# Kernel tuning notes

Measured on AMD Instinct MI355X. Metric: run time of the kernel, lower is better.

## Reference

```python
import jax, jax.numpy as jnp
import numpy as np
from jax import lax

MAX_DISP = 192
DOWNSAMPLE = 4
DEPTH = MAX_DISP // DOWNSAMPLE  # 48 disparity levels
B, C, H, W = 4, 512, 96, 320


def setup_inputs() -> dict:
    key = jax.random.key(0)
    k1, k2 = jax.random.split(key)
    left_features = jax.random.normal(k1, (B, C, H, W), dtype=jnp.float32)
    right_features = jax.random.normal(k2, (B, C, H, W), dtype=jnp.float32)
    return {"left_features": left_features, "right_features": right_features}


def _cost_volume(left, right):
    # cost[b, i, h, w] = mean_c left[b,c,h,w] * right[b,c,h,w-i]  for w >= i, else 0
    w_idx = jnp.arange(left.shape[3])

    def body(carry, i):
        r = jnp.roll(right, i, axis=3)            # right[..., w-i] (wrapped)
        corr = jnp.mean(left * r, axis=1)         # [B, H, W]
        corr = jnp.where(w_idx >= i, corr, jnp.float32(0.0))
        return carry, corr

    _, cost = lax.scan(body, None, jnp.arange(DEPTH))  # [D, B, H, W]
    return jnp.transpose(cost, (1, 0, 2, 3))           # [B, D, H, W]


def reference(left_features, right_features):
    return _cost_volume(left_features, right_features)
```

## Files before the change

kernel.cpp:

```cpp
#include <hip/hip_runtime.h>
#include <hip/hip_bf16.h>

#define B_ 4
#define C_ 512
#define H_ 96
#define W_ 320
#define D_ 48
#define HW_ (H_*W_)

#define KC 32
#define NCHUNK (C_/KC)
#define LCOLS 160
#define COLS 368
#define CSTR 72
#define BUFB (COLS*CSTR)
#define NT 320
#define NC4 (COLS/4)
#define NU (NC4*8)
#define SIT 3
#define EPS 168

typedef __attribute__((ext_vector_type(8))) short bf16x8;
typedef __attribute__((ext_vector_type(4))) float f32x4;

__device__ __forceinline__ unsigned cvt2(float lo, float hi) {
  union { __hip_bfloat162 h2; unsigned u; } u;
  u.h2 = __float22bfloat162_rn(make_float2(lo, hi));
  return u.u;
}
__device__ __forceinline__ int ldsoff(int col, int q) {
  return col * CSTR + (q << 3);
}

#define BAR() do { \
  asm volatile("s_waitcnt lgkmcnt(0)" ::: "memory"); \
  __builtin_amdgcn_sched_barrier(0); \
  __builtin_amdgcn_s_barrier(); \
  __builtin_amdgcn_sched_barrier(0); } while (0)

__global__ __launch_bounds__(NT, 4)
void cost_volume_mfma(const float* __restrict__ Lp,
                      const float* __restrict__ Rp,
                      float* __restrict__ out) {
  __shared__ __align__(16) char lds[2 * BUFB];
  const int tid = threadIdx.x;
  const int bid = blockIdx.x;
  const int half = bid & 1;
  const int bh = bid >> 1;
  const int b = bh / H_, h = bh % H_;
  const int wv = tid >> 6;
  const int lc = tid & 15;
  const int lg = (tid >> 4) & 3;
  const int mh0 = 2 * wv;
  const int m0 = 10 * half + mh0;

  const float* sp[SIT];
  int dstb[SIT];
  bool sact[SIT];
#pragma unroll
  for (int it = 0; it < SIT; ++it) {
    const int u = tid + NT * it;
    bool a = (u < NU);
    const int uc = a ? u : 0;
    const int c4 = uc % NC4;
    const int chq = uc / NC4;
    const int col = 4 * c4;
    int x;
    const float* basep;
    if (col < LCOLS) { x = 160 * half + col; basep = Lp; }
    else             { x = 160 * half - 48 + (col - LCOLS); basep = Rp; a = a && (x >= 0); }
    if (x < 0) x = 0;
    sp[it] = basep + ((size_t)(b * C_ + 4 * chq) * H_ + h) * W_ + x;
    dstb[it] = ldsoff(col, chq);
    sact[it] = a;
  }

  float4 sreg[SIT][4];

#define SLOAD() \
  _Pragma("unroll") for (int it = 0; it < SIT; ++it) { \
    if (sact[it]) { \
      _Pragma("unroll") for (int l = 0; l < 4; ++l) \
        sreg[it][l] = *(const float4*)(sp[it] + (size_t)l * HW_); \
    } \
    sp[it] += (size_t)KC * HW_; \
  }

#define SWRITE(bb) \
  _Pragma("unroll") for (int it = 0; it < SIT; ++it) if (sact[it]) { \
    char* p = lds + (bb) * BUFB + dstb[it]; \
    uint2 v; \
    v.x = cvt2(sreg[it][0].x, sreg[it][1].x); v.y = cvt2(sreg[it][2].x, sreg[it][3].x); \
    *(uint2*)(p) = v; \
    v.x = cvt2(sreg[it][0].y, sreg[it][1].y); v.y = cvt2(sreg[it][2].y, sreg[it][3].y); \
    *(uint2*)(p + CSTR) = v; \
    v.x = cvt2(sreg[it][0].z, sreg[it][1].z); v.y = cvt2(sreg[it][2].z, sreg[it][3].z); \
    *(uint2*)(p + 2 * CSTR) = v; \
    v.x = cvt2(sreg[it][0].w, sreg[it][1].w); v.y = cvt2(sreg[it][2].w, sreg[it][3].w); \
    *(uint2*)(p + 3 * CSTR) = v; \
  }

  const int aoff0 = ldsoff(16 * mh0 + lc, 2 * lg);
  const int aoff1 = ldsoff(16 * (mh0 + 1) + lc, 2 * lg);
  int boff[5];
  bool bval[5];
#pragma unroll
  for (int dnp = 0; dnp < 5; ++dnp) {
    const int jn = m0 + 1 - dnp;
    const int jloc = jn - 10 * half;
    boff[dnp] = ldsoff(208 + 16 * jloc + lc, 2 * lg);
    bval[dnp] = (jn >= 0);
  }

  union FragU { uint2 h[2]; bf16x8 v; };
#define FREAD(fr, base, off) do { FragU _f; \
  _f.h[0] = *(const uint2*)((base) + (off)); \
  _f.h[1] = *(const uint2*)((base) + (off) + 8); fr = _f.v; } while (0)

  f32x4 acc[2][4];
#pragma unroll
  for (int ml = 0; ml < 2; ++ml)
#pragma unroll
    for (int dn = 0; dn < 4; ++dn) acc[ml][dn] = (f32x4){0.f, 0.f, 0.f, 0.f};

  SLOAD();
  SWRITE(0);
  SLOAD();
  BAR();
#pragma unroll 2
  for (int k = 0; k < NCHUNK; ++k) {
    const char* base = lds + (k & 1) * BUFB;
    bf16x8 a0, a1;
    FREAD(a0, base, aoff0);
    FREAD(a1, base, aoff1);
    bf16x8 bf[5];
#pragma unroll
    for (int dnp = 0; dnp < 5; ++dnp)
      if (bval[dnp]) FREAD(bf[dnp], base, boff[dnp]);
#pragma unroll
    for (int dn = 0; dn < 4; ++dn) {
      if (bval[dn + 1])
        acc[0][dn] = __builtin_amdgcn_mfma_f32_16x16x32_bf16(a0, bf[dn + 1], acc[0][dn], 0, 0, 0);
      if (bval[dn])
        acc[1][dn] = __builtin_amdgcn_mfma_f32_16x16x32_bf16(a1, bf[dn], acc[1][dn], 0, 0, 0);
    }
    if (k < NCHUNK - 1) {
      SWRITE((k + 1) & 1);
      if (k < NCHUNK - 2) SLOAD();
      BAR();
    }
  }

  __syncthreads();
  float* ep = (float*)lds;
#pragma unroll
  for (int e = 0; e < (D_ * EPS + NT - 1) / NT; ++e) {
    const int i = tid + NT * e;
    if (i < D_ * EPS) ep[i] = 0.f;
  }
  __syncthreads();
  const float scale = 1.f / 512.f;
#pragma unroll
  for (int ml = 0; ml < 2; ++ml) {
    const int mh = mh0 + ml;
#pragma unroll
    for (int dn = 0; dn < 4; ++dn) {
      const int jn = m0 + ml - dn;
      if (jn >= 0) {
#pragma unroll
        for (int q = 0; q < 4; ++q) {
          const int i = 4 * lg + q;
          const int d = 16 * dn + i - lc;
          if (d >= 0 && d < D_)
            ep[d * EPS + 16 * mh + i] = acc[ml][dn][q] * scale;
        }
      }
    }
  }
  __syncthreads();
#pragma unroll
  for (int e = 0; e < 6; ++e) {
    const int u = tid + NT * e;
    const int d = u / 40, c4 = u % 40;
    const float4 v = *(const float4*)(ep + d * EPS + 4 * c4);
    float* o = out + (((size_t)b * D_ + d) * H_ + h) * W_ + 160 * half + 4 * c4;
    *(float4*)o = v;
  }
}

extern "C" void kernel_launch(void* const* d_in, const int* in_sizes, int n_in,
                              void* d_out, int out_size, void* d_ws, size_t ws_size,
                              hipStream_t stream) {
  const float* left  = (const float*)d_in[0];
  const float* right = (const float*)d_in[1];
  float* outp = (float*)d_out;
  cost_volume_mfma<<<dim3(B_ * H_ * 2), dim3(NT), 0, stream>>>(left, right, outp);
}
```

Baseline: 124.4 us.

## Double-buffer global prefetch registers to fetch two chunks ahead

Adds a second register staging set so global loads run two channel chunks ahead, alternating between two register buffers. The shared-memory write of the next chunk is moved before the MFMA work of the current chunk, and the launch bound drops from 4 to 3 blocks per CU to free registers. The aim is to hide more HBM latency in what is mostly a bandwidth-bound loop. In exchange, register pressure rises and fewer blocks may be resident per CU.

After: 154.6 us. 24.2% more time.

```diff
diff --git a/kernel.cpp b/kernel.cpp
--- a/kernel.cpp
+++ b/kernel.cpp
@@ -38,7 +38,7 @@
   __builtin_amdgcn_s_barrier(); \
   __builtin_amdgcn_sched_barrier(0); } while (0)
 
-__global__ __launch_bounds__(NT, 4)
+__global__ __launch_bounds__(NT, 3)
 void cost_volume_mfma(const float* __restrict__ Lp,
                       const float* __restrict__ Rp,
                       float* __restrict__ out) {
@@ -54,7 +54,8 @@
   const int mh0 = 2 * wv;
   const int m0 = 10 * half + mh0;
 
-  const float* sp[SIT];
+  const float* spA[SIT];
+  const float* spB[SIT];
   int dstb[SIT];
   bool sact[SIT];
 #pragma unroll
@@ -70,33 +71,34 @@
     if (col < LCOLS) { x = 160 * half + col; basep = Lp; }
     else             { x = 160 * half - 48 + (col - LCOLS); basep = Rp; a = a && (x >= 0); }
     if (x < 0) x = 0;
-    sp[it] = basep + ((size_t)(b * C_ + 4 * chq) * H_ + h) * W_ + x;
+    spA[it] = basep + ((size_t)(b * C_ + 4 * chq) * H_ + h) * W_ + x;
+    spB[it] = spA[it] + (size_t)2 * KC * HW_;
     dstb[it] = ldsoff(col, chq);
     sact[it] = a;
   }
 
-  float4 sreg[SIT][4];
-
-#define SLOAD() \
+  float4 srA[SIT][4], srB[SIT][4];
+
+#define SLOADX(sr, sp, ADVCH) \
   _Pragma("unroll") for (int it = 0; it < SIT; ++it) { \
     if (sact[it]) { \
       _Pragma("unroll") for (int l = 0; l < 4; ++l) \
-        sreg[it][l] = *(const float4*)(sp[it] + (size_t)l * HW_); \
+        sr[it][l] = *(const float4*)(sp[it] + (size_t)l * HW_); \
     } \
-    sp[it] += (size_t)KC * HW_; \
-  }
-
-#define SWRITE(bb) \
+    sp[it] += (size_t)(ADVCH) * KC * HW_; \
+  }
+
+#define SWRITEX(sr, bb) \
   _Pragma("unroll") for (int it = 0; it < SIT; ++it) if (sact[it]) { \
     char* p = lds + (bb) * BUFB + dstb[it]; \
     uint2 v; \
-    v.x = cvt2(sreg[it][0].x, sreg[it][1].x); v.y = cvt2(sreg[it][2].x, sreg[it][3].x); \
+    v.x = cvt2(sr[it][0].x, sr[it][1].x); v.y = cvt2(sr[it][2].x, sr[it][3].x); \
     *(uint2*)(p) = v; \
-    v.x = cvt2(sreg[it][0].y, sreg[it][1].y); v.y = cvt2(sreg[it][2].y, sreg[it][3].y); \
+    v.x = cvt2(sr[it][0].y, sr[it][1].y); v.y = cvt2(sr[it][2].y, sr[it][3].y); \
     *(uint2*)(p + CSTR) = v; \
-    v.x = cvt2(sreg[it][0].z, sreg[it][1].z); v.y = cvt2(sreg[it][2].z, sreg[it][3].z); \
+    v.x = cvt2(sr[it][0].z, sr[it][1].z); v.y = cvt2(sr[it][2].z, sr[it][3].z); \
     *(uint2*)(p + 2 * CSTR) = v; \
-    v.x = cvt2(sreg[it][0].w, sreg[it][1].w); v.y = cvt2(sreg[it][2].w, sreg[it][3].w); \
+    v.x = cvt2(sr[it][0].w, sr[it][1].w); v.y = cvt2(sr[it][2].w, sr[it][3].w); \
     *(uint2*)(p + 3 * CSTR) = v; \
   }
 
@@ -123,12 +125,23 @@
 #pragma unroll
     for (int dn = 0; dn < 4; ++dn) acc[ml][dn] = (f32x4){0.f, 0.f, 0.f, 0.f};
 
-  SLOAD();
-  SWRITE(0);
-  SLOAD();
+  SLOADX(srA, spA, 1);
+  SWRITEX(srA, 0);
+  SLOADX(srA, spA, 2);
+  SLOADX(srB, spB, 2);
   BAR();
+
 #pragma unroll 2
   for (int k = 0; k < NCHUNK; ++k) {
+    if (k < NCHUNK - 1) {
+      if ((k & 1) == 0) {
+        SWRITEX(srA, (k + 1) & 1);
+        if (k < NCHUNK - 3) SLOADX(srA, spA, 2);
+      } else {
+        SWRITEX(srB, (k + 1) & 1);
+        if (k < NCHUNK - 3) SLOADX(srB, spB, 2);
+      }
+    }
     const char* base = lds + (k & 1) * BUFB;
     bf16x8 a0, a1;
     FREAD(a0, base, aoff0);
@@ -144,11 +157,7 @@
       if (bval[dn])
         acc[1][dn] = __builtin_amdgcn_mfma_f32_16x16x32_bf16(a1, bf[dn], acc[1][dn], 0, 0, 0);
     }
-    if (k < NCHUNK - 1) {
-      SWRITE((k + 1) & 1);
-      if (k < NCHUNK - 2) SLOAD();
-      BAR();
-    }
+    if (k < NCHUNK - 1) BAR();
   }
 
   __syncthreads();
```

## Split each row into single-wave blocks with private LDS windows and no barriers

Applied to the files above, without the earlier changes.

Each block is now one 64-thread wave that owns a 32-column output tile, up from 320-thread blocks each covering half a row. The launch grows to ten blocks per (batch, row). Each wave stages its own left tile plus the 80-column right window it needs into a single LDS buffer, so the double buffer and the workgroup barriers go away. The aim is more resident waves and no cross-wave synchronisation. The cost is that right-feature columns are loaded redundantly by neighbouring tiles, raising global/L2 traffic, and there is less explicit load/compute overlap per wave.

Measured after the change: 142.3 us. 1.14x slower.

```diff
diff --git a/kernel.cpp b/kernel.cpp
--- a/kernel.cpp
+++ b/kernel.cpp
@@ -10,15 +10,13 @@
 
 #define KC 32
 #define NCHUNK (C_/KC)
-#define LCOLS 160
-#define COLS 368
+#define WCOLS 112
 #define CSTR 72
-#define BUFB (COLS*CSTR)
-#define NT 320
-#define NC4 (COLS/4)
-#define NU (NC4*8)
-#define SIT 3
-#define EPS 168
+#define LDSB (WCOLS*CSTR)
+#define NT 64
+#define NUW 224
+#define SIT 4
+#define EPS2 36
 
 typedef __attribute__((ext_vector_type(8))) short bf16x8;
 typedef __attribute__((ext_vector_type(4))) float f32x4;
@@ -32,45 +30,41 @@
   return col * CSTR + (q << 3);
 }
 
-#define BAR() do { \
-  asm volatile("s_waitcnt lgkmcnt(0)" ::: "memory"); \
-  __builtin_amdgcn_sched_barrier(0); \
-  __builtin_amdgcn_s_barrier(); \
-  __builtin_amdgcn_sched_barrier(0); } while (0)
-
-__global__ __launch_bounds__(NT, 4)
+__global__ __launch_bounds__(NT)
 void cost_volume_mfma(const float* __restrict__ Lp,
                       const float* __restrict__ Rp,
                       float* __restrict__ out) {
-  __shared__ __align__(16) char lds[2 * BUFB];
-  const int tid = threadIdx.x;
+  __shared__ __align__(16) char lds[LDSB];
+  const int ln = threadIdx.x;
   const int bid = blockIdx.x;
-  const int half = bid & 1;
-  const int bh = bid >> 1;
+  const int t2 = bid % 10;
+  const int bh = bid / 10;
   const int b = bh / H_, h = bh % H_;
-  const int wv = tid >> 6;
-  const int lc = tid & 15;
-  const int lg = (tid >> 4) & 3;
-  const int mh0 = 2 * wv;
-  const int m0 = 10 * half + mh0;
+  const int lc = ln & 15;
+  const int lg = (ln >> 4) & 3;
+  const int m0 = 2 * t2;
 
   const float* sp[SIT];
   int dstb[SIT];
   bool sact[SIT];
 #pragma unroll
   for (int it = 0; it < SIT; ++it) {
-    const int u = tid + NT * it;
-    bool a = (u < NU);
+    const int u = ln + 64 * it;
+    bool a = (u < NUW);
     const int uc = a ? u : 0;
-    const int c4 = uc % NC4;
-    const int chq = uc / NC4;
+    const int c4 = uc % 28, chq = uc / 28;
     const int col = 4 * c4;
     int x;
-    const float* basep;
-    if (col < LCOLS) { x = 160 * half + col; basep = Lp; }
-    else             { x = 160 * half - 48 + (col - LCOLS); basep = Rp; a = a && (x >= 0); }
+    const float* bp;
+    if (c4 < 8) { x = 16 * m0 + col; bp = Lp; }
+    else {
+      const int dnp = (c4 - 8) >> 2, jn = m0 + 1 - dnp;
+      x = 16 * jn + 4 * ((c4 - 8) & 3);
+      bp = Rp;
+      a = a && (jn >= 0);
+    }
     if (x < 0) x = 0;
-    sp[it] = basep + ((size_t)(b * C_ + 4 * chq) * H_ + h) * W_ + x;
+    sp[it] = bp + ((size_t)(b * C_ + 4 * chq) * H_ + h) * W_ + x;
     dstb[it] = ldsoff(col, chq);
     sact[it] = a;
   }
@@ -86,9 +80,9 @@
     sp[it] += (size_t)KC * HW_; \
   }
 
-#define SWRITE(bb) \
+#define SWRITE() \
   _Pragma("unroll") for (int it = 0; it < SIT; ++it) if (sact[it]) { \
-    char* p = lds + (bb) * BUFB + dstb[it]; \
+    char* p = lds + dstb[it]; \
     uint2 v; \
     v.x = cvt2(sreg[it][0].x, sreg[it][1].x); v.y = cvt2(sreg[it][2].x, sreg[it][3].x); \
     *(uint2*)(p) = v; \
@@ -100,22 +94,20 @@
     *(uint2*)(p + 3 * CSTR) = v; \
   }
 
-  const int aoff0 = ldsoff(16 * mh0 + lc, 2 * lg);
-  const int aoff1 = ldsoff(16 * (mh0 + 1) + lc, 2 * lg);
+  const int aoff0 = ldsoff(lc, 2 * lg);
+  const int aoff1 = ldsoff(16 + lc, 2 * lg);
   int boff[5];
   bool bval[5];
 #pragma unroll
   for (int dnp = 0; dnp < 5; ++dnp) {
-    const int jn = m0 + 1 - dnp;
-    const int jloc = jn - 10 * half;
-    boff[dnp] = ldsoff(208 + 16 * jloc + lc, 2 * lg);
-    bval[dnp] = (jn >= 0);
+    boff[dnp] = ldsoff(32 + 16 * dnp + lc, 2 * lg);
+    bval[dnp] = (m0 + 1 - dnp) >= 0;
   }
 
   union FragU { uint2 h[2]; bf16x8 v; };
-#define FREAD(fr, base, off) do { FragU _f; \
-  _f.h[0] = *(const uint2*)((base) + (off)); \
-  _f.h[1] = *(const uint2*)((base) + (off) + 8); fr = _f.v; } while (0)
+#define FREAD(fr, off) do { FragU _f; \
+  _f.h[0] = *(const uint2*)(lds + (off)); \
+  _f.h[1] = *(const uint2*)(lds + (off) + 8); fr = _f.v; } while (0)
 
   f32x4 acc[2][4];
 #pragma unroll
@@ -124,19 +116,16 @@
     for (int dn = 0; dn < 4; ++dn) acc[ml][dn] = (f32x4){0.f, 0.f, 0.f, 0.f};
 
   SLOAD();
-  SWRITE(0);
+  SWRITE();
   SLOAD();
-  BAR();
-#pragma unroll 2
   for (int k = 0; k < NCHUNK; ++k) {
-    const char* base = lds + (k & 1) * BUFB;
     bf16x8 a0, a1;
-    FREAD(a0, base, aoff0);
-    FREAD(a1, base, aoff1);
+    FREAD(a0, aoff0);
+    FREAD(a1, aoff1);
     bf16x8 bf[5];
 #pragma unroll
     for (int dnp = 0; dnp < 5; ++dnp)
-      if (bval[dnp]) FREAD(bf[dnp], base, boff[dnp]);
+      if (bval[dnp]) FREAD(bf[dnp], boff[dnp]);
 #pragma unroll
     for (int dn = 0; dn < 4; ++dn) {
       if (bval[dn + 1])
@@ -144,35 +133,30 @@
       if (bval[dn])
         acc[1][dn] = __builtin_amdgcn_mfma_f32_16x16x32_bf16(a1, bf[dn], acc[1][dn], 0, 0, 0);
     }
-    if (k < NCHUNK - 1) {
-      SWRITE((k + 1) & 1);
-      if (k < NCHUNK - 2) SLOAD();
-      BAR();
-    }
+    if (k < NCHUNK - 1) SWRITE();
+    if (k < NCHUNK - 2) SLOAD();
   }
 
   __syncthreads();
   float* ep = (float*)lds;
 #pragma unroll
-  for (int e = 0; e < (D_ * EPS + NT - 1) / NT; ++e) {
-    const int i = tid + NT * e;
-    if (i < D_ * EPS) ep[i] = 0.f;
+  for (int e = 0; e < (D_ * EPS2 + NT - 1) / NT; ++e) {
+    const int i = ln + NT * e;
+    if (i < D_ * EPS2) ep[i] = 0.f;
   }
   __syncthreads();
   const float scale = 1.f / 512.f;
 #pragma unroll
   for (int ml = 0; ml < 2; ++ml) {
-    const int mh = mh0 + ml;
 #pragma unroll
     for (int dn = 0; dn < 4; ++dn) {
-      const int jn = m0 + ml - dn;
-      if (jn >= 0) {
+      if ((m0 + ml - dn) >= 0) {
 #pragma unroll
         for (int q = 0; q < 4; ++q) {
           const int i = 4 * lg + q;
           const int d = 16 * dn + i - lc;
           if (d >= 0 && d < D_)
-            ep[d * EPS + 16 * mh + i] = acc[ml][dn][q] * scale;
+            ep[d * EPS2 + 16 * ml + i] = acc[ml][dn][q] * scale;
         }
       }
     }
@@ -180,10 +164,10 @@
   __syncthreads();
 #pragma unroll
   for (int e = 0; e < 6; ++e) {
-    const int u = tid + NT * e;
-    const int d = u / 40, c4 = u % 40;
-    const float4 v = *(const float4*)(ep + d * EPS + 4 * c4);
-    float* o = out + (((size_t)b * D_ + d) * H_ + h) * W_ + 160 * half + 4 * c4;
+    const int u = ln + NT * e;
+    const int d = u >> 3, c4 = u & 7;
+    const float4 v = *(const float4*)(ep + d * EPS2 + 4 * c4);
+    float* o = out + (((size_t)b * D_ + d) * H_ + h) * W_ + 16 * m0 + 4 * c4;
     *(float4*)o = v;
   }
 }
@@ -194,5 +178,5 @@
   const float* left  = (const float*)d_in[0];
   const float* right = (const float*)d_in[1];
   float* outp = (float*)d_out;
-  cost_volume_mfma<<<dim3(B_ * H_ * 2), dim3(NT), 0, stream>>>(left, right, outp);
+  cost_volume_mfma<<<dim3(B_ * H_ * 10), dim3(NT), 0, stream>>>(left, right, outp);
 }
```
